# Performance work log

Measured on AMD Instinct MI355X. Metric: run time of the kernel, lower is better.

Reference implementation:

```python
import jax, jax.numpy as jnp
import numpy as np

N_SRC = 50000
N_DST1 = 20000
N_DST2 = 10000
E1 = 320000
E2 = 160000
T = 12
C_IN = 64
HID = 16
C_OUT = 32


def _gat_layer(src_feat, dst_feat, src_idx, dst_idx, ew, W, a_l, a_r, n_dst):
    # src_feat: [N_src, T, C], dst_feat: [N_dst, T, C]
    h_src = jnp.einsum('ntc,co->nto', src_feat, W)   # [N_src, T, O]
    h_dst = jnp.einsum('ntc,co->nto', dst_feat, W)   # [N_dst, T, O]
    el = jnp.einsum('nto,o->nt', h_src, a_l)          # [N_src, T]
    er = jnp.einsum('nto,o->nt', h_dst, a_r)          # [N_dst, T]
    # per-edge attention logits
    e = jax.nn.leaky_relu(el[src_idx] + er[dst_idx], negative_slope=0.2)  # [E, T]
    # segment softmax over incoming edges of each dst node
    m = jax.ops.segment_max(e, dst_idx, num_segments=n_dst)               # [N_dst, T]
    ex = jnp.exp(e - m[dst_idx])
    s = jax.ops.segment_sum(ex, dst_idx, num_segments=n_dst)
    alpha = ex / (s[dst_idx] + 1e-9)                                      # [E, T]
    msg = (alpha * ew[:, None])[:, :, None] * h_src[src_idx]              # [E, T, O]
    return jax.ops.segment_sum(msg, dst_idx, num_segments=n_dst)          # [N_dst, T, O]


def setup_inputs() -> dict:
    key = jax.random.key(0)
    ks = jax.random.split(key, 12)
    inp = {
        'node_feat': jax.random.normal(ks[0], (T, N_SRC, C_IN), dtype=jnp.float32),
        'edge_src1': jax.random.randint(ks[1], (E1,), 0, N_SRC, dtype=jnp.int32),
        'edge_dst1': jax.random.randint(ks[2], (E1,), 0, N_DST1, dtype=jnp.int32),
        'edge_weight1': jax.random.uniform(ks[3], (E1,), dtype=jnp.float32),
        'edge_src2': jax.random.randint(ks[4], (E2,), 0, N_DST1, dtype=jnp.int32),
        'edge_dst2': jax.random.randint(ks[5], (E2,), 0, N_DST2, dtype=jnp.int32),
        'edge_weight2': jax.random.uniform(ks[6], (E2,), dtype=jnp.float32),
        'W1': jax.random.normal(ks[7], (C_IN, HID), dtype=jnp.float32) * (1.0 / np.sqrt(C_IN)),
        'a_l1': jax.random.normal(ks[8], (HID,), dtype=jnp.float32) * 0.1,
        'a_r1': jax.random.normal(ks[9], (HID,), dtype=jnp.float32) * 0.1,
        'W2': jax.random.normal(ks[10], (HID, C_OUT), dtype=jnp.float32) * (1.0 / np.sqrt(HID)),
        'a_l2': jax.random.normal(ks[11], (C_OUT,), dtype=jnp.float32) * 0.1,
        'a_r2': jax.random.normal(jax.random.fold_in(key, 99), (C_OUT,), dtype=jnp.float32) * 0.1,
    }
    return inp


def reference(node_feat, edge_src1, edge_dst1, edge_weight1,
              edge_src2, edge_dst2, edge_weight2,
              W1, a_l1, a_r1, W2, a_l2, a_r2):
    # [T, N, C] -> [N, T, C]
    x = jnp.transpose(node_feat, (1, 0, 2))
    h1 = _gat_layer(x, x[:N_DST1], edge_src1, edge_dst1, edge_weight1,
                    W1, a_l1, a_r1, N_DST1)
    h1 = jax.nn.leaky_relu(h1, negative_slope=0.01)
    h2 = _gat_layer(h1, h1[:N_DST2], edge_src2, edge_dst2, edge_weight2,
                    W2, a_l2, a_r2, N_DST2)
    h2 = jax.nn.leaky_relu(h2, negative_slope=0.01)
    # [N_dst2, T, O] -> [T, N_dst2, O]
    return jnp.transpose(h2, (1, 0, 2))
```

## Files before the change

### kernel.cpp

```cpp
#include <hip/hip_runtime.h>

#define N_SRC 50000
#define N_DST1 20000
#define N_DST2 10000
#define E1 320000
#define E2 160000
#define T 12
#define C_IN 64
#define HID 16
#define C_OUT 32

__device__ __forceinline__ float lrelu(float x, float s) { return x > 0.f ? x : s * x; }

__device__ __forceinline__ int xcd_swizzle(int p, int W) {
    int x = p & 7, k = p >> 3;
    int q = W >> 3, r = W & 7;
    return (x < r ? x * (q + 1) : r * (q + 1) + (x - r) * q) + k;
}

__global__ __launch_bounds__(256) void k_transform1(
    const float* __restrict__ nf, const float* __restrict__ W1,
    const float* __restrict__ a_l, const float* __restrict__ a_r,
    float* __restrict__ hs1, float* __restrict__ el1, float* __restrict__ er1)
{
    __shared__ float xs[64][68];
    __shared__ float w[C_IN][HID];
    __shared__ float al[HID], ar[HID];
    int tx = threadIdx.x;
    int t = blockIdx.y;
    int n0 = blockIdx.x * 64;
    int nrem = N_SRC - n0; if (nrem > 64) nrem = 64;

    reinterpret_cast<float4*>(&w[0][0])[tx] = reinterpret_cast<const float4*>(W1)[tx];
    if (tx < HID) al[tx] = a_l[tx];
    else if (tx < 2 * HID) ar[tx - HID] = a_r[tx - HID];

    const float4* gp = reinterpret_cast<const float4*>(nf + ((size_t)t * N_SRC + n0) * C_IN);
#pragma unroll
    for (int k = 0; k < 4; k++) {
        int f = k * 256 + tx;
        int node = f >> 4;
        if (node < nrem)
            *reinterpret_cast<float4*>(&xs[node][(f & 15) * 4]) = gp[f];
    }
    __syncthreads();

    int q = tx & 3;
    int nn = tx >> 2;
    float4 acc = make_float4(0.f, 0.f, 0.f, 0.f);
#pragma unroll
    for (int c4 = 0; c4 < 16; c4++) {
        float4 xA = *reinterpret_cast<const float4*>(&xs[nn][c4 * 4]);
        float4 w0 = *reinterpret_cast<const float4*>(&w[c4 * 4 + 0][q * 4]);
        float4 w1 = *reinterpret_cast<const float4*>(&w[c4 * 4 + 1][q * 4]);
        float4 w2 = *reinterpret_cast<const float4*>(&w[c4 * 4 + 2][q * 4]);
        float4 w3 = *reinterpret_cast<const float4*>(&w[c4 * 4 + 3][q * 4]);
        acc.x += xA.x * w0.x + xA.y * w1.x + xA.z * w2.x + xA.w * w3.x;
        acc.y += xA.x * w0.y + xA.y * w1.y + xA.z * w2.y + xA.w * w3.y;
        acc.z += xA.x * w0.z + xA.y * w1.z + xA.z * w2.z + xA.w * w3.z;
        acc.w += xA.x * w0.w + xA.y * w1.w + xA.z * w2.w + xA.w * w3.w;
    }

    float el = acc.x * al[q * 4] + acc.y * al[q * 4 + 1] + acc.z * al[q * 4 + 2] + acc.w * al[q * 4 + 3];
    float er = acc.x * ar[q * 4] + acc.y * ar[q * 4 + 1] + acc.z * ar[q * 4 + 2] + acc.w * ar[q * 4 + 3];
    el += __shfl_xor(el, 1); el += __shfl_xor(el, 2);
    er += __shfl_xor(er, 1); er += __shfl_xor(er, 2);

    if (nn < nrem) {
        float* hb = hs1 + ((size_t)t * N_SRC + n0) * HID;
        *reinterpret_cast<float4*>(hb + (size_t)nn * HID + q * 4) = acc;
        if (q == 0) {
            int n = n0 + nn;
            el1[(size_t)t * N_SRC + n] = el;
            if (n < N_DST1) er1[(size_t)t * N_DST1 + n] = er;
        }
    }
}

__global__ __launch_bounds__(1024) void k_csr(
    const int* __restrict__ d1, const int* __restrict__ d2,
    int* __restrict__ off1, int* __restrict__ cur1,
    int* __restrict__ off2, int* __restrict__ cur2,
    const float* __restrict__ W2, const float* __restrict__ al2,
    const float* __restrict__ ar2, float* __restrict__ wl2, float* __restrict__ wr2)
{
    __shared__ int cnt[N_DST1];
    __shared__ int part[1024];
    int tx = threadIdx.x;
    if (blockIdx.x == 2) {
        if (tx < 32) {
            int c = tx & 15;
            const float* a = (tx < 16) ? al2 : ar2;
            float s = 0.f;
            for (int o = 0; o < C_OUT; o++) s += W2[c * C_OUT + o] * a[o];
            if (tx < 16) wl2[c] = s; else wr2[c] = s;
        }
        return;
    }
    const int* dst = (blockIdx.x == 0) ? d1 : d2;
    int E = (blockIdx.x == 0) ? E1 : E2;
    int N = (blockIdx.x == 0) ? N_DST1 : N_DST2;
    int* off = (blockIdx.x == 0) ? off1 : off2;
    int* cur = (blockIdx.x == 0) ? cur1 : cur2;

    for (int i = tx; i < N; i += 1024) cnt[i] = 0;
    __syncthreads();
    for (int e = tx; e < E; e += 1024) atomicAdd(&cnt[dst[e]], 1);
    __syncthreads();

    int CH = (N + 1023) / 1024;
    int base = tx * CH;
    int p = 0;
    for (int k = 0; k < CH; k++) { int i = base + k; if (i < N) p += cnt[i]; }
    part[tx] = p;
    __syncthreads();
#pragma unroll
    for (int dd = 1; dd < 1024; dd <<= 1) {
        int v = (tx >= dd) ? part[tx - dd] : 0;
        __syncthreads();
        part[tx] += v;
        __syncthreads();
    }
    int run = (tx == 0) ? 0 : part[tx - 1];
    if (tx == 0) off[0] = 0;
    for (int k = 0; k < CH; k++) {
        int i = base + k;
        if (i < N) { cur[i] = run; run += cnt[i]; off[i + 1] = run; }
    }
}

__global__ __launch_bounds__(256) void k_scatter(
    const int* __restrict__ s1, const int* __restrict__ d1, const float* __restrict__ w1,
    int* __restrict__ cur1, int2* __restrict__ sw1,
    const int* __restrict__ s2, const int* __restrict__ d2, const float* __restrict__ w2,
    int* __restrict__ cur2, int2* __restrict__ sw2)
{
    int e = blockIdx.x * 256 + threadIdx.x;
    if (e < E1) {
        int d = d1[e];
        int p = atomicAdd(&cur1[d], 1);
        sw1[p] = make_int2(s1[e], __float_as_int(w1[e]));
    } else if (e < E1 + E2) {
        int ee = e - E1;
        int d = d2[ee];
        int p = atomicAdd(&cur2[d], 1);
        sw2[p] = make_int2(s2[ee], __float_as_int(w2[ee]));
    }
}

template <int NDST, int NSRC, bool FINAL>
__global__ __launch_bounds__(256) void k_gat(
    const int* __restrict__ off, const int2* __restrict__ sw,
    const float* __restrict__ el, const float* __restrict__ er,
    const float* __restrict__ hs, float* __restrict__ outp,
    const float* __restrict__ wl, const float* __restrict__ wr,
    float* __restrict__ el_out, float* __restrict__ er_out)
{
    __shared__ float w2s[FINAL ? HID * C_OUT : 1];
    int tx = threadIdx.x;
    if (FINAL) {
        for (int idx = tx; idx < HID * C_OUT; idx += 256) w2s[idx] = wl[idx];
        __syncthreads();
    }
    int wblk = xcd_swizzle(blockIdx.x, (NDST * T) / 16);
    int grp = tx >> 4;
    int lane16 = tx & 15;
    int q = lane16 & 3;
    int eslot = lane16 >> 2;
    int g = wblk * 16 + grp;
    int t = g / NDST;
    int d = g - t * NDST;
    int start = off[d], end = off[d + 1];
    float erv = er[g];
    const float* elb = el + (size_t)t * NSRC;
    const float* hsb = hs + (size_t)t * NSRC * HID;

    float4 num = make_float4(0.f, 0.f, 0.f, 0.f);
    float den = 0.f;
    int i = start + eslot;
    for (; i + 4 < end; i += 8) {
        int2 sa = sw[i];
        int2 sb = sw[i + 4];
        float ea = elb[sa.x];
        float eb = elb[sb.x];
        float4 ha = *reinterpret_cast<const float4*>(hsb + (size_t)sa.x * HID + q * 4);
        float4 hb = *reinterpret_cast<const float4*>(hsb + (size_t)sb.x * HID + q * 4);
        float exa = __expf(lrelu(ea + erv, 0.2f));
        float exb = __expf(lrelu(eb + erv, 0.2f));
        den += exa + exb;
        float ca = exa * __int_as_float(sa.y);
        float cb = exb * __int_as_float(sb.y);
        num.x += ca * ha.x + cb * hb.x;
        num.y += ca * ha.y + cb * hb.y;
        num.z += ca * ha.z + cb * hb.z;
        num.w += ca * ha.w + cb * hb.w;
    }
    if (i < end) {
        int2 sa = sw[i];
        float ea = elb[sa.x];
        float4 ha = *reinterpret_cast<const float4*>(hsb + (size_t)sa.x * HID + q * 4);
        float exa = __expf(lrelu(ea + erv, 0.2f));
        den += exa;
        float ca = exa * __int_as_float(sa.y);
        num.x += ca * ha.x; num.y += ca * ha.y;
        num.z += ca * ha.z; num.w += ca * ha.w;
    }
#pragma unroll
    for (int mk = 4; mk <= 8; mk <<= 1) {
        num.x += __shfl_xor(num.x, mk);
        num.y += __shfl_xor(num.y, mk);
        num.z += __shfl_xor(num.z, mk);
        num.w += __shfl_xor(num.w, mk);
        den   += __shfl_xor(den, mk);
    }
    float inv = 1.f / (den + 1e-9f);
    float4 v = make_float4(num.x * inv, num.y * inv, num.z * inv, num.w * inv);

    if (!FINAL) {
        v.x = lrelu(v.x, 0.01f); v.y = lrelu(v.y, 0.01f);
        v.z = lrelu(v.z, 0.01f); v.w = lrelu(v.w, 0.01f);
        if (eslot == 0) {
            *reinterpret_cast<float4*>(outp + (size_t)g * HID + q * 4) = v;
            float pl = v.x * wl[q * 4] + v.y * wl[q * 4 + 1] + v.z * wl[q * 4 + 2] + v.w * wl[q * 4 + 3];
            float pr = v.x * wr[q * 4] + v.y * wr[q * 4 + 1] + v.z * wr[q * 4 + 2] + v.w * wr[q * 4 + 3];
            pl += __shfl_xor(pl, 1); pl += __shfl_xor(pl, 2);
            pr += __shfl_xor(pr, 1); pr += __shfl_xor(pr, 2);
            if (q == 0) {
                el_out[g] = pl;
                if (d < N_DST2) er_out[(size_t)t * N_DST2 + d] = pr;
            }
        }
    } else {
        float4 v1, v2, v3;
        v1.x = __shfl_xor(v.x, 1); v1.y = __shfl_xor(v.y, 1); v1.z = __shfl_xor(v.z, 1); v1.w = __shfl_xor(v.w, 1);
        v2.x = __shfl_xor(v.x, 2); v2.y = __shfl_xor(v.y, 2); v2.z = __shfl_xor(v.z, 2); v2.w = __shfl_xor(v.w, 2);
        v3.x = __shfl_xor(v.x, 3); v3.y = __shfl_xor(v.y, 3); v3.z = __shfl_xor(v.z, 3); v3.w = __shfl_xor(v.w, 3);
        int obase = q * 8;
        float out8[8];
#pragma unroll
        for (int oo = 0; oo < 8; oo++) out8[oo] = 0.f;
#define ACCQ(Q, R0)                                                             \
        {                                                                       \
            int r0 = (R0) * 4;                                                  \
            _Pragma("unroll")                                                   \
            for (int oo = 0; oo < 8; oo++)                                      \
                out8[oo] += (Q).x * w2s[(r0 + 0) * C_OUT + obase + oo]          \
                          + (Q).y * w2s[(r0 + 1) * C_OUT + obase + oo]          \
                          + (Q).z * w2s[(r0 + 2) * C_OUT + obase + oo]          \
                          + (Q).w * w2s[(r0 + 3) * C_OUT + obase + oo];         \
        }
        ACCQ(v,  q);
        ACCQ(v1, q ^ 1);
        ACCQ(v2, q ^ 2);
        ACCQ(v3, q ^ 3);
#undef ACCQ
        if (eslot == 0) {
            float* op = outp + (size_t)g * C_OUT + obase;
            float4 w0 = make_float4(lrelu(out8[0], 0.01f), lrelu(out8[1], 0.01f),
                                    lrelu(out8[2], 0.01f), lrelu(out8[3], 0.01f));
            float4 w1 = make_float4(lrelu(out8[4], 0.01f), lrelu(out8[5], 0.01f),
                                    lrelu(out8[6], 0.01f), lrelu(out8[7], 0.01f));
            *reinterpret_cast<float4*>(op) = w0;
            *reinterpret_cast<float4*>(op + 4) = w1;
        }
    }
}

extern "C" void kernel_launch(void* const* d_in, const int* in_sizes, int n_in,
                              void* d_out, int out_size, void* d_ws, size_t ws_size,
                              hipStream_t stream)
{
    const float* node_feat = (const float*)d_in[0];
    const int*   esrc1     = (const int*)d_in[1];
    const int*   edst1     = (const int*)d_in[2];
    const float* ew1       = (const float*)d_in[3];
    const int*   esrc2     = (const int*)d_in[4];
    const int*   edst2     = (const int*)d_in[5];
    const float* ew2       = (const float*)d_in[6];
    const float* W1        = (const float*)d_in[7];
    const float* a_l1      = (const float*)d_in[8];
    const float* a_r1      = (const float*)d_in[9];
    const float* W2        = (const float*)d_in[10];
    const float* a_l2      = (const float*)d_in[11];
    const float* a_r2      = (const float*)d_in[12];
    float* out = (float*)d_out;

    float* ws = (float*)d_ws;
    float* hs1 = ws;
    float* el1 = hs1 + 9600000;
    float* er1 = el1 + 600000;
    float* h1  = er1 + 240000;
    float* el2 = h1 + 3840000;
    float* er2 = el2 + 240000;
    float* wl2 = er2 + 120000;
    float* wr2 = wl2 + 16;
    int2* sw1 = (int2*)(wr2 + 16);
    int2* sw2 = sw1 + E1;
    int* off1 = (int*)(sw2 + E2);
    int* cur1 = off1 + N_DST1 + 1;
    int* off2 = cur1 + N_DST1;
    int* cur2 = off2 + N_DST2 + 1;

    k_csr<<<3, 1024, 0, stream>>>(edst1, edst2, off1, cur1, off2, cur2,
                                  W2, a_l2, a_r2, wl2, wr2);
    k_scatter<<<(E1 + E2 + 255) / 256, 256, 0, stream>>>(
        esrc1, edst1, ew1, cur1, sw1,
        esrc2, edst2, ew2, cur2, sw2);

    {
        dim3 g((N_SRC + 63) / 64, T);
        k_transform1<<<g, 256, 0, stream>>>(node_feat, W1, a_l1, a_r1, hs1, el1, er1);
    }
    k_gat<N_DST1, N_SRC, false><<<(N_DST1 * T) / 16, 256, 0, stream>>>(
        off1, sw1, el1, er1, hs1, h1, wl2, wr2, el2, er2);
    k_gat<N_DST2, N_DST1, true><<<(N_DST2 * T) / 16, 256, 0, stream>>>(
        off2, sw2, el2, er2, h1, out, W2, nullptr, nullptr, nullptr);
}
```

Before: 249.2 us.

## Split CSR build into grid-wide histogram, zeroing, and single-block scan kernels

The old CSR build ran the destination-degree histogram inside a single 1024-thread block per graph, so 320k atomic adds were serialized on one CU. The new code zeroes global count arrays, builds the histogram with a full grid of global atomics, then runs the prefix scan in a small kernel that reads counts from global memory. This spreads the histogram across the whole GPU. In exchange it adds two kernel launches and uses global rather than LDS atomics.

```diff
diff --git a/kernel.cpp b/kernel.cpp
--- a/kernel.cpp
+++ b/kernel.cpp
@@ -16,6 +16,12 @@
     int x = p & 7, k = p >> 3;
     int q = W >> 3, r = W & 7;
     return (x < r ? x * (q + 1) : r * (q + 1) + (x - r) * q) + k;
+}
+
+__global__ __launch_bounds__(256) void k_zero(int4* __restrict__ p, int n4)
+{
+    int i = blockIdx.x * 256 + threadIdx.x;
+    if (i < n4) p[i] = make_int4(0, 0, 0, 0);
 }
 
 __global__ __launch_bounds__(256) void k_transform1(
@@ -77,17 +83,48 @@
     }
 }
 
-__global__ __launch_bounds__(1024) void k_csr(
+__global__ __launch_bounds__(256) void k_hist(
     const int* __restrict__ d1, const int* __restrict__ d2,
-    int* __restrict__ off1, int* __restrict__ cur1,
-    int* __restrict__ off2, int* __restrict__ cur2,
+    int* __restrict__ cnt1, int* __restrict__ cnt2)
+{
+    int e = blockIdx.x * 256 + threadIdx.x;
+    if (e < E1) atomicAdd(&cnt1[d1[e]], 1);
+    else if (e < E1 + E2) atomicAdd(&cnt2[d2[e - E1]], 1);
+}
+
+__device__ void scan_one(const int* cnt, int* off, int* cur, int N)
+{
+    __shared__ int part[1024];
+    int tx = threadIdx.x;
+    int CH = (N + 1023) / 1024;
+    int base = tx * CH;
+    int p = 0;
+    for (int k = 0; k < CH; k++) { int i = base + k; if (i < N) p += cnt[i]; }
+    part[tx] = p;
+    __syncthreads();
+#pragma unroll
+    for (int d = 1; d < 1024; d <<= 1) {
+        int v = (tx >= d) ? part[tx - d] : 0;
+        __syncthreads();
+        part[tx] += v;
+        __syncthreads();
+    }
+    int run = (tx == 0) ? 0 : part[tx - 1];
+    if (tx == 0) off[0] = 0;
+    for (int k = 0; k < CH; k++) {
+        int i = base + k;
+        if (i < N) { cur[i] = run; run += cnt[i]; off[i + 1] = run; }
+    }
+}
+
+__global__ __launch_bounds__(1024) void k_scan(
+    const int* __restrict__ cnt1, int* __restrict__ off1, int* __restrict__ cur1,
+    const int* __restrict__ cnt2, int* __restrict__ off2, int* __restrict__ cur2,
     const float* __restrict__ W2, const float* __restrict__ al2,
     const float* __restrict__ ar2, float* __restrict__ wl2, float* __restrict__ wr2)
 {
-    __shared__ int cnt[N_DST1];
-    __shared__ int part[1024];
-    int tx = threadIdx.x;
     if (blockIdx.x == 2) {
+        int tx = threadIdx.x;
         if (tx < 32) {
             int c = tx & 15;
             const float* a = (tx < 16) ? al2 : ar2;
@@ -97,36 +134,8 @@
         }
         return;
     }
-    const int* dst = (blockIdx.x == 0) ? d1 : d2;
-    int E = (blockIdx.x == 0) ? E1 : E2;
-    int N = (blockIdx.x == 0) ? N_DST1 : N_DST2;
-    int* off = (blockIdx.x == 0) ? off1 : off2;
-    int* cur = (blockIdx.x == 0) ? cur1 : cur2;
-
-    for (int i = tx; i < N; i += 1024) cnt[i] = 0;
-    __syncthreads();
-    for (int e = tx; e < E; e += 1024) atomicAdd(&cnt[dst[e]], 1);
-    __syncthreads();
-
-    int CH = (N + 1023) / 1024;
-    int base = tx * CH;
-    int p = 0;
-    for (int k = 0; k < CH; k++) { int i = base + k; if (i < N) p += cnt[i]; }
-    part[tx] = p;
-    __syncthreads();
-#pragma unroll
-    for (int dd = 1; dd < 1024; dd <<= 1) {
-        int v = (tx >= dd) ? part[tx - dd] : 0;
-        __syncthreads();
-        part[tx] += v;
-        __syncthreads();
-    }
-    int run = (tx == 0) ? 0 : part[tx - 1];
-    if (tx == 0) off[0] = 0;
-    for (int k = 0; k < CH; k++) {
-        int i = base + k;
-        if (i < N) { cur[i] = run; run += cnt[i]; off[i + 1] = run; }
-    }
+    if (blockIdx.x == 0) scan_one(cnt1, off1, cur1, N_DST1);
+    else                 scan_one(cnt2, off2, cur2, N_DST2);
 }
 
 __global__ __launch_bounds__(256) void k_scatter(
@@ -296,13 +305,17 @@
     float* wr2 = wl2 + 16;
     int2* sw1 = (int2*)(wr2 + 16);
     int2* sw2 = sw1 + E1;
-    int* off1 = (int*)(sw2 + E2);
+    int* cnt1 = (int*)(sw2 + E2);
+    int* cnt2 = cnt1 + N_DST1;
+    int* off1 = cnt2 + N_DST2;
     int* cur1 = off1 + N_DST1 + 1;
     int* off2 = cur1 + N_DST1;
     int* cur2 = off2 + N_DST2 + 1;
 
-    k_csr<<<3, 1024, 0, stream>>>(edst1, edst2, off1, cur1, off2, cur2,
-                                  W2, a_l2, a_r2, wl2, wr2);
+    k_zero<<<30, 256, 0, stream>>>((int4*)cnt1, (N_DST1 + N_DST2) / 4);
+    k_hist<<<(E1 + E2 + 255) / 256, 256, 0, stream>>>(edst1, edst2, cnt1, cnt2);
+    k_scan<<<3, 1024, 0, stream>>>(cnt1, off1, cur1, cnt2, off2, cur2,
+                                   W2, a_l2, a_r2, wl2, wr2);
     k_scatter<<<(E1 + E2 + 255) / 256, 256, 0, stream>>>(
         esrc1, edst1, ew1, cur1, sw1,
         esrc2, edst2, ew2, cur2, sw2);
```

Measured after the change: 209.2 us. -16.0%, faster.
